# Kernel optimization log

Measured on AMD Instinct MI355X. Metric: run time of the kernel, lower is better.

The kernel has to match this reference:

```python
import jax, jax.numpy as jnp
import numpy as np

L, B, D = 2048, 8, 1024
EPS = 1e-5


def setup_inputs() -> dict:
    key = jax.random.key(0)
    k1, k2 = jax.random.split(key)
    x = jax.random.normal(k1, (L, B, D), dtype=jnp.float32)
    c = jnp.zeros((B, D), dtype=jnp.float32)
    # w_ufr: Linear(D, 3D); weight init normal(std=0.001), bias zero except
    # the reset-gate third which is filled with 2.0 (per the torch init).
    W = jax.random.normal(k2, (3 * D, D), dtype=jnp.float32) * 0.001
    b = jnp.zeros((3 * D,), dtype=jnp.float32).at[2 * D:].set(2.0)
    gamma = jnp.ones((D,), dtype=jnp.float32)
    beta = jnp.zeros((D,), dtype=jnp.float32)
    return {"x": x, "c": c, "W": W, "b": b, "gamma": gamma, "beta": beta}


def _layernorm(x, gamma, beta):
    mu = jnp.mean(x, axis=-1, keepdims=True)
    var = jnp.var(x, axis=-1, keepdims=True)
    return (x - mu) * jax.lax.rsqrt(var + EPS) * gamma + beta


def reference(x, c, W, b, gamma, beta):
    residual = x
    x_norm = _layernorm(x, gamma, beta)            # [L,B,D]
    ufr = jnp.einsum('lbd,ed->lbe', x_norm, W) + b  # [L,B,3D]
    u, f, r = jnp.split(ufr, 3, axis=-1)
    f_gate = jax.nn.sigmoid(f)
    r_gate = jax.nn.sigmoid(r)

    def step(c_prev, fu):
        f_t, u_t = fu
        c_t = f_t * c_prev + (1.0 - f_t) * u_t
        return c_t, c_t

    last_c, c_stack = jax.lax.scan(step, c, (f_gate, u))  # c_stack: [L,B,D]
    hs = r_gate * jnp.tanh(c_stack) + (1.0 - r_gate) * x_norm
    # dropout is identity in eval mode
    return residual + hs, last_c
```

## Files before the change

### kernel.cpp

```cpp
#include <hip/hip_runtime.h>
#include <hip/hip_bf16.h>

#define L_DIM 2048
#define B_DIM 8
#define D_DIM 1024
#define M_DIM (L_DIM * B_DIM)
#define N_DIM (3 * D_DIM)
#define K_DIM D_DIM
#define BD (B_DIM * D_DIM)
#define NCHUNK 64
#define CLEN (L_DIM / NCHUNK)

typedef __attribute__((ext_vector_type(8))) __bf16 bf16x8;
typedef __attribute__((ext_vector_type(4))) __bf16 bf16x4;
typedef __attribute__((ext_vector_type(4))) float f32x4;

#define GLOAD_LDS16(g, l)                                        \
  __builtin_amdgcn_global_load_lds(                              \
      (const __attribute__((address_space(1))) void*)(g),        \
      (__attribute__((address_space(3))) void*)(l), 16, 0, 0)

__device__ __forceinline__ float sigmoidf_(float v) {
  return 1.0f / (1.0f + __expf(-v));
}

__global__ __launch_bounds__(256) void ln_kernel(
    const float* __restrict__ x, const float* __restrict__ gamma,
    const float* __restrict__ beta, __bf16* __restrict__ xn) {
  const int row = blockIdx.x;
  const int tid = threadIdx.x;
  const float4 v = ((const float4*)(x + (size_t)row * D_DIM))[tid];
  float s  = v.x + v.y + v.z + v.w;
  float ss = v.x * v.x + v.y * v.y + v.z * v.z + v.w * v.w;
  #pragma unroll
  for (int off = 32; off > 0; off >>= 1) {
    s  += __shfl_xor(s, off);
    ss += __shfl_xor(ss, off);
  }
  __shared__ float sb[8];
  const int wid = tid >> 6, lane = tid & 63;
  if (lane == 0) { sb[wid] = s; sb[4 + wid] = ss; }
  __syncthreads();
  const float tot  = sb[0] + sb[1] + sb[2] + sb[3];
  const float tot2 = sb[4] + sb[5] + sb[6] + sb[7];
  const float mu  = tot * (1.0f / D_DIM);
  const float var = tot2 * (1.0f / D_DIM) - mu * mu;
  const float rstd = rsqrtf(var + 1e-5f);
  const float4 g  = ((const float4*)gamma)[tid];
  const float4 bt = ((const float4*)beta)[tid];
  bf16x4 o;
  o[0] = (__bf16)((v.x - mu) * rstd * g.x + bt.x);
  o[1] = (__bf16)((v.y - mu) * rstd * g.y + bt.y);
  o[2] = (__bf16)((v.z - mu) * rstd * g.z + bt.z);
  o[3] = (__bf16)((v.w - mu) * rstd * g.w + bt.w);
  ((bf16x4*)(xn + (size_t)row * D_DIM))[tid] = o;
}

__global__ __launch_bounds__(256) void wconv_kernel(
    const float* __restrict__ W, __bf16* __restrict__ Wb) {
  const size_t i = ((size_t)blockIdx.x * 256 + threadIdx.x) * 4;
  const float4 v = *(const float4*)(W + i);
  bf16x4 o;
  o[0] = (__bf16)v.x; o[1] = (__bf16)v.y; o[2] = (__bf16)v.z; o[3] = (__bf16)v.w;
  *(bf16x4*)(Wb + i) = o;
}

#define VMCNT(n) asm volatile("s_waitcnt vmcnt(" #n ")" ::: "memory")

__global__ __launch_bounds__(512, 2) void gemm256_kernel(
    const __bf16* __restrict__ A,
    const __bf16* __restrict__ Bm,
    const float* __restrict__ bias,
    __bf16* __restrict__ U, __bf16* __restrict__ FG, __bf16* __restrict__ RG) {
  __shared__ __bf16 lds[65536];
  const int tid = threadIdx.x;
  const int lane = tid & 63;
  const int wid = tid >> 6;
  const int wm = wid >> 2;
  const int wn = wid & 3;
  const int g  = wn >> 1;

  const int bid0 = blockIdx.x;
  const int bid = (bid0 & 7) * 96 + (bid0 >> 3);
  const int bm = bid / 12, bn = bid % 12;

  const int arow0 = bm * 256 + wm * 128;
  const int brow0 = bn * 256 + g * 128;
  const int akg = wn;
  const int bkg = wm * 2 + (wn & 1);

#define AUNIT(buf, half, ks) ((buf) * 32768 + (half) * 8192 + (ks) * 4096)
#define BUNIT(buf, gg, ks)   ((buf) * 32768 + 16384 + (gg) * 8192 + (ks) * 4096)

  auto stageA = [&](int kt2, int ks) {
    const int buf = kt2 & 1;
    const __bf16* gs = A + (size_t)arow0 * K_DIM + kt2 * 64 + ks * 32 + akg * 8;
    __bf16* ls = lds + AUNIT(buf, wm, ks) + akg * 1024;
    GLOAD_LDS16(gs + (size_t)lane * K_DIM, ls + lane * 8);
    GLOAD_LDS16(gs + (size_t)(lane + 64) * K_DIM, ls + (lane + 64) * 8);
  };
  auto stageB = [&](int kt2, int ks) {
    const int buf = kt2 & 1;
    const __bf16* gs = Bm + (size_t)brow0 * K_DIM + kt2 * 64 + ks * 32 + bkg * 8;
    __bf16* ls = lds + BUNIT(buf, g, ks) + bkg * 1024;
    GLOAD_LDS16(gs + (size_t)lane * K_DIM, ls + lane * 8);
    GLOAD_LDS16(gs + (size_t)(lane + 64) * K_DIM, ls + (lane + 64) * 8);
  };

  const int fr = lane & 15, fk = lane >> 4;
  auto rdA = [&](int buf, int ks, int m) {
    return *(const bf16x8*)(lds + AUNIT(buf, wm, ks) + fk * 1024 +
                            (m * 16 + fr) * 8);
  };
  auto rdB = [&](int buf, int ks, int n) {
    return *(const bf16x8*)(lds + BUNIT(buf, g, ks) + fk * 1024 +
                            ((wn & 1) * 64 + n * 16 + fr) * 8);
  };

  f32x4 acc[8][4] = {};

  stageA(0, 0); stageB(0, 0); stageA(0, 1); stageB(0, 1);
  stageA(1, 0); stageB(1, 0);
  VMCNT(4);
  __builtin_amdgcn_s_barrier();

  #pragma unroll 1
  for (int kt = 0; kt < 16; ++kt) {
    const int buf = kt & 1;
    bf16x8 a[4], b[4];

    #pragma unroll
    for (int m = 0; m < 4; ++m) a[m] = rdA(buf, 0, m);
    #pragma unroll
    for (int n = 0; n < 4; ++n) b[n] = rdB(buf, 0, n);
    if (kt < 15) stageA(kt + 1, 1);
    __builtin_amdgcn_s_barrier();
    __builtin_amdgcn_s_setprio(1);
    #pragma unroll
    for (int m = 0; m < 4; ++m)
      #pragma unroll
      for (int n = 0; n < 4; ++n)
        acc[m][n] = __builtin_amdgcn_mfma_f32_16x16x32_bf16(a[m], b[n],
                                                            acc[m][n], 0, 0, 0);
    __builtin_amdgcn_s_setprio(0);
    __builtin_amdgcn_s_barrier();

    #pragma unroll
    for (int m = 0; m < 4; ++m) a[m] = rdA(buf, 0, m + 4);
    if (kt < 15) stageB(kt + 1, 1);
    __builtin_amdgcn_s_barrier();
    __builtin_amdgcn_s_setprio(1);
    #pragma unroll
    for (int m = 0; m < 4; ++m)
      #pragma unroll
      for (int n = 0; n < 4; ++n)
        acc[m + 4][n] = __builtin_amdgcn_mfma_f32_16x16x32_bf16(
            a[m], b[n], acc[m + 4][n], 0, 0, 0);
    __builtin_amdgcn_s_setprio(0);
    if (kt == 15) { VMCNT(0); } else { VMCNT(8); }
    __builtin_amdgcn_s_barrier();

    #pragma unroll
    for (int m = 0; m < 4; ++m) a[m] = rdA(buf, 1, m);
    #pragma unroll
    for (int n = 0; n < 4; ++n) b[n] = rdB(buf, 1, n);
    if (kt < 14) stageA(kt + 2, 0);
    __builtin_amdgcn_s_barrier();
    __builtin_amdgcn_s_setprio(1);
    #pragma unroll
    for (int m = 0; m < 4; ++m)
      #pragma unroll
      for (int n = 0; n < 4; ++n)
        acc[m][n] = __builtin_amdgcn_mfma_f32_16x16x32_bf16(a[m], b[n],
                                                            acc[m][n], 0, 0, 0);
    __builtin_amdgcn_s_setprio(0);
    __builtin_amdgcn_s_barrier();

    #pragma unroll
    for (int m = 0; m < 4; ++m) a[m] = rdA(buf, 1, m + 4);
    if (kt < 14) stageB(kt + 2, 0);
    __builtin_amdgcn_s_barrier();
    __builtin_amdgcn_s_setprio(1);
    #pragma unroll
    for (int m = 0; m < 4; ++m)
      #pragma unroll
      for (int n = 0; n < 4; ++n)
        acc[m + 4][n] = __builtin_amdgcn_mfma_f32_16x16x32_bf16(
            a[m], b[n], acc[m + 4][n], 0, 0, 0);
    __builtin_amdgcn_s_setprio(0);
    if (kt < 14) { VMCNT(8); }
    else if (kt == 14) { VMCNT(4); }
    __builtin_amdgcn_s_barrier();
  }

  const int seg = bn >> 2;
  __bf16* outb = (seg == 0) ? U : ((seg == 1) ? FG : RG);
  const int nl0 = (bn & 3) * 256 + wn * 64;
  const int m00 = bm * 256 + wm * 128;
  #pragma unroll
  for (int n = 0; n < 4; ++n) {
    const int col = nl0 + n * 16 + fr;
    const float bv = bias[seg * 1024 + col];
    #pragma unroll
    for (int m = 0; m < 8; ++m) {
      const int r0 = m00 + m * 16 + fk * 4;
      #pragma unroll
      for (int j = 0; j < 4; ++j) {
        float v = acc[m][n][j] + bv;
        if (seg != 0) v = sigmoidf_(v);
        outb[(size_t)(r0 + j) * D_DIM + col] = (__bf16)v;
      }
    }
  }
}

__global__ __launch_bounds__(256) void scanA_kernel(
    const __bf16* __restrict__ fg, const __bf16* __restrict__ u,
    float* __restrict__ av) {
  const int ci = blockIdx.x;
  const int bd = blockIdx.y * 256 + threadIdx.x;
  float a = 1.0f, v = 0.0f;
  const size_t base = (size_t)ci * CLEN * BD + bd;
  #pragma unroll 8
  for (int i = 0; i < CLEN; ++i) {
    const size_t idx = base + (size_t)i * BD;
    const float f = (float)fg[idx];
    const float uu = (float)u[idx];
    a *= f;
    v = f * v + (1.0f - f) * uu;
  }
  av[(size_t)ci * BD + bd] = a;
  av[(size_t)NCHUNK * BD + (size_t)ci * BD + bd] = v;
}

__global__ __launch_bounds__(256) void scanB_kernel(
    const float* __restrict__ av, const float* __restrict__ c0,
    float* __restrict__ carries, float* __restrict__ out1) {
  const int bd = blockIdx.x * 256 + threadIdx.x;
  float c = c0[bd];
  #pragma unroll 8
  for (int ci = 0; ci < NCHUNK; ++ci) {
    carries[(size_t)ci * BD + bd] = c;
    c = av[(size_t)ci * BD + bd] * c + av[(size_t)NCHUNK * BD + (size_t)ci * BD + bd];
  }
  out1[bd] = c;
}

__global__ __launch_bounds__(256) void scanC_kernel(
    const __bf16* __restrict__ fg, const __bf16* __restrict__ u,
    const __bf16* __restrict__ rg, const __bf16* __restrict__ xn,
    const float* __restrict__ x, const float* __restrict__ carries,
    float* __restrict__ out0) {
  const int ci = blockIdx.x;
  const int bd = blockIdx.y * 256 + threadIdx.x;
  float c = carries[(size_t)ci * BD + bd];
  const size_t base = (size_t)ci * CLEN * BD + bd;
  #pragma unroll 4
  for (int i = 0; i < CLEN; ++i) {
    const size_t idx = base + (size_t)i * BD;
    const float f = (float)fg[idx];
    const float uu = (float)u[idx];
    c = f * c + (1.0f - f) * uu;
    const float r = (float)rg[idx];
    const float xnv = (float)xn[idx];
    const float hs = r * tanhf(c) + (1.0f - r) * xnv;
    out0[idx] = x[idx] + hs;
  }
}

extern "C" void kernel_launch(void* const* d_in, const int* in_sizes, int n_in,
                              void* d_out, int out_size, void* d_ws,
                              size_t ws_size, hipStream_t stream) {
  const float* x     = (const float*)d_in[0];
  const float* c0    = (const float*)d_in[1];
  const float* W     = (const float*)d_in[2];
  const float* bias  = (const float*)d_in[3];
  const float* gamma = (const float*)d_in[4];
  const float* beta  = (const float*)d_in[5];

  float* out0 = (float*)d_out;
  float* out1 = out0 + (size_t)M_DIM * D_DIM;

  char* ws = (char*)d_ws;
  __bf16* xn = (__bf16*)(ws + 0);
  __bf16* Wb = (__bf16*)(ws + 33554432);
  __bf16* U  = (__bf16*)(ws + 39845888);
  __bf16* FG = (__bf16*)(ws + 73400320);
  __bf16* RG = (__bf16*)(ws + 106954752);
  float* av      = (float*)(ws + 140509184);
  float* carries = (float*)(ws + 144703488);

  ln_kernel<<<M_DIM, 256, 0, stream>>>(x, gamma, beta, xn);
  wconv_kernel<<<(N_DIM * K_DIM / 4) / 256, 256, 0, stream>>>(W, Wb);
  gemm256_kernel<<<(M_DIM / 256) * (N_DIM / 256), 512, 0, stream>>>(
      xn, Wb, bias, U, FG, RG);
  scanA_kernel<<<dim3(NCHUNK, BD / 256), 256, 0, stream>>>(FG, U, av);
  scanB_kernel<<<BD / 256, 256, 0, stream>>>(av, c0, carries, out1);
  scanC_kernel<<<dim3(NCHUNK, BD / 256), 256, 0, stream>>>(
      FG, U, RG, xn, x, carries, out0);
}
```

Baseline: 241.6 us.

## Swizzle GEMM LDS layout for row-contiguous loads and stage epilogue through LDS

Global-to-LDS staging is changed so each thread loads a 16-byte piece of a row, with the k-slot XOR-swizzled by row. This makes global reads row-contiguous instead of strided per lane, and the fragment reads use the matching swizzle to avoid LDS bank conflicts. The epilogue now writes the bias+sigmoid results into padded LDS one half-tile at a time, then emits 16-byte coalesced global stores instead of scattered 2-byte stores. The cost is extra barriers and an LDS round trip in the epilogue.

```diff
diff --git a/kernel.cpp b/kernel.cpp
--- a/kernel.cpp
+++ b/kernel.cpp
@@ -78,49 +78,44 @@
   const int wid = tid >> 6;
   const int wm = wid >> 2;
   const int wn = wid & 3;
-  const int g  = wn >> 1;
+  const int g2 = wn >> 1;
 
   const int bid0 = blockIdx.x;
   const int bid = (bid0 & 7) * 96 + (bid0 >> 3);
   const int bm = bid / 12, bn = bid % 12;
 
-  const int arow0 = bm * 256 + wm * 128;
-  const int brow0 = bn * 256 + g * 128;
-  const int akg = wn;
-  const int bkg = wm * 2 + (wn & 1);
-
-#define AUNIT(buf, half, ks) ((buf) * 32768 + (half) * 8192 + (ks) * 4096)
-#define BUNIT(buf, gg, ks)   ((buf) * 32768 + 16384 + (gg) * 8192 + (ks) * 4096)
-
-  auto stageA = [&](int kt2, int ks) {
-    const int buf = kt2 & 1;
-    const __bf16* gs = A + (size_t)arow0 * K_DIM + kt2 * 64 + ks * 32 + akg * 8;
-    __bf16* ls = lds + AUNIT(buf, wm, ks) + akg * 1024;
-    GLOAD_LDS16(gs + (size_t)lane * K_DIM, ls + lane * 8);
-    GLOAD_LDS16(gs + (size_t)(lane + 64) * K_DIM, ls + (lane + 64) * 8);
+#define AUNIT(buf, h, ks) ((buf) * 32768 + (h) * 8192 + (ks) * 4096)
+#define BUNIT(buf, h, ks) ((buf) * 32768 + 16384 + (h) * 8192 + (ks) * 4096)
+
+  const int srow  = tid >> 2;
+  const int sslot = (tid & 3) ^ ((srow >> 1) & 3);
+  auto stageA = [&](int kt2, int h, int ks) {
+    const __bf16* gs = A + (size_t)(bm * 256 + h * 128 + srow) * K_DIM +
+                       kt2 * 64 + ks * 32 + sslot * 8;
+    GLOAD_LDS16(gs, lds + AUNIT(kt2 & 1, h, ks) + tid * 8);
   };
-  auto stageB = [&](int kt2, int ks) {
-    const int buf = kt2 & 1;
-    const __bf16* gs = Bm + (size_t)brow0 * K_DIM + kt2 * 64 + ks * 32 + bkg * 8;
-    __bf16* ls = lds + BUNIT(buf, g, ks) + bkg * 1024;
-    GLOAD_LDS16(gs + (size_t)lane * K_DIM, ls + lane * 8);
-    GLOAD_LDS16(gs + (size_t)(lane + 64) * K_DIM, ls + (lane + 64) * 8);
+  auto stageB = [&](int kt2, int h, int ks) {
+    const __bf16* gs = Bm + (size_t)(bn * 256 + h * 128 + srow) * K_DIM +
+                       kt2 * 64 + ks * 32 + sslot * 8;
+    GLOAD_LDS16(gs, lds + BUNIT(kt2 & 1, h, ks) + tid * 8);
   };
 
   const int fr = lane & 15, fk = lane >> 4;
+  const int swz = fk ^ ((fr >> 1) & 3);
   auto rdA = [&](int buf, int ks, int m) {
-    return *(const bf16x8*)(lds + AUNIT(buf, wm, ks) + fk * 1024 +
-                            (m * 16 + fr) * 8);
+    return *(const bf16x8*)(lds + AUNIT(buf, wm, ks) + (m * 16 + fr) * 32 +
+                            swz * 8);
   };
   auto rdB = [&](int buf, int ks, int n) {
-    return *(const bf16x8*)(lds + BUNIT(buf, g, ks) + fk * 1024 +
-                            ((wn & 1) * 64 + n * 16 + fr) * 8);
+    return *(const bf16x8*)(lds + BUNIT(buf, g2, ks) +
+                            ((wn & 1) * 64 + n * 16 + fr) * 32 + swz * 8);
   };
 
   f32x4 acc[8][4] = {};
 
-  stageA(0, 0); stageB(0, 0); stageA(0, 1); stageB(0, 1);
-  stageA(1, 0); stageB(1, 0);
+  stageA(0, 0, 0); stageA(0, 1, 0); stageB(0, 0, 0); stageB(0, 1, 0);
+  stageA(0, 0, 1); stageA(0, 1, 1); stageB(0, 0, 1); stageB(0, 1, 1);
+  stageA(1, 0, 0); stageA(1, 1, 0); stageB(1, 0, 0); stageB(1, 1, 0);
   VMCNT(4);
   __builtin_amdgcn_s_barrier();
 
@@ -133,7 +128,7 @@
     for (int m = 0; m < 4; ++m) a[m] = rdA(buf, 0, m);
     #pragma unroll
     for (int n = 0; n < 4; ++n) b[n] = rdB(buf, 0, n);
-    if (kt < 15) stageA(kt + 1, 1);
+    if (kt < 15) { stageA(kt + 1, 0, 1); stageA(kt + 1, 1, 1); }
     __builtin_amdgcn_s_barrier();
     __builtin_amdgcn_s_setprio(1);
     #pragma unroll
@@ -147,7 +142,7 @@
 
     #pragma unroll
     for (int m = 0; m < 4; ++m) a[m] = rdA(buf, 0, m + 4);
-    if (kt < 15) stageB(kt + 1, 1);
+    if (kt < 15) { stageB(kt + 1, 0, 1); stageB(kt + 1, 1, 1); }
     __builtin_amdgcn_s_barrier();
     __builtin_amdgcn_s_setprio(1);
     #pragma unroll
@@ -164,7 +159,7 @@
     for (int m = 0; m < 4; ++m) a[m] = rdA(buf, 1, m);
     #pragma unroll
     for (int n = 0; n < 4; ++n) b[n] = rdB(buf, 1, n);
-    if (kt < 14) stageA(kt + 2, 0);
+    if (kt < 14) { stageA(kt + 2, 0, 0); stageA(kt + 2, 1, 0); }
     __builtin_amdgcn_s_barrier();
     __builtin_amdgcn_s_setprio(1);
     #pragma unroll
@@ -178,7 +173,7 @@
 
     #pragma unroll
     for (int m = 0; m < 4; ++m) a[m] = rdA(buf, 1, m + 4);
-    if (kt < 14) stageB(kt + 2, 0);
+    if (kt < 14) { stageB(kt + 2, 0, 0); stageB(kt + 2, 1, 0); }
     __builtin_amdgcn_s_barrier();
     __builtin_amdgcn_s_setprio(1);
     #pragma unroll
@@ -195,21 +190,38 @@
 
   const int seg = bn >> 2;
   __bf16* outb = (seg == 0) ? U : ((seg == 1) ? FG : RG);
-  const int nl0 = (bn & 3) * 256 + wn * 64;
-  const int m00 = bm * 256 + wm * 128;
+  const int segcol0 = (bn & 3) * 256;
+
+  float bv[4];
   #pragma unroll
-  for (int n = 0; n < 4; ++n) {
-    const int col = nl0 + n * 16 + fr;
-    const float bv = bias[seg * 1024 + col];
-    #pragma unroll
-    for (int m = 0; m < 8; ++m) {
-      const int r0 = m00 + m * 16 + fk * 4;
-      #pragma unroll
-      for (int j = 0; j < 4; ++j) {
-        float v = acc[m][n][j] + bv;
-        if (seg != 0) v = sigmoidf_(v);
-        outb[(size_t)(r0 + j) * D_DIM + col] = (__bf16)v;
-      }
+  for (int n = 0; n < 4; ++n)
+    bv[n] = bias[seg * 1024 + segcol0 + wn * 64 + n * 16 + fr];
+
+  const int lrow = tid >> 5;
+  const int chunk = tid & 31;
+  #pragma unroll 1
+  for (int h = 0; h < 2; ++h) {
+    __syncthreads();
+    if (wm == h) {
+      #pragma unroll
+      for (int m = 0; m < 8; ++m)
+        #pragma unroll
+        for (int n = 0; n < 4; ++n)
+          #pragma unroll
+          for (int j = 0; j < 4; ++j) {
+            float v = acc[m][n][j] + bv[n];
+            if (seg != 0) v = sigmoidf_(v);
+            lds[(m * 16 + fk * 4 + j) * 264 + wn * 64 + n * 16 + fr] =
+                (__bf16)v;
+          }
+    }
+    __syncthreads();
+    #pragma unroll
+    for (int it = 0; it < 8; ++it) {
+      const int r = it * 16 + lrow;
+      const bf16x8 val = *(const bf16x8*)(lds + r * 264 + chunk * 8);
+      const size_t grow = (size_t)(bm * 256 + h * 128 + r);
+      *(bf16x8*)(outb + grow * D_DIM + segcol0 + chunk * 8) = val;
     }
   }
 }
```

New measurement: 231.8 us. -4.0%, faster.
